# Optimization experiments

Measured on AMD Instinct MI355X. Metric: run time of the kernel, lower is better.

## Reference

```python
import jax, jax.numpy as jnp
import numpy as np

N_NODES = 20000
N_EDGES = 320000
C = 64  # classes
NEG_SLOPE = 0.2  # DGL GATConv default


def setup_inputs() -> dict:
    key = jax.random.key(0)
    ks = jax.random.split(key, 32)
    dims = [C, 2 * C, 4 * C, 8 * C, 16 * C]
    inp = {}
    inp["feat"] = jax.random.normal(ks[0], (N_NODES, C), jnp.float32)
    k = 1
    for i in range(4):
        din, dout = dims[i], dims[i + 1]
        scale = 1.0 / np.sqrt(din)
        inp[f"W{i+1}"] = jax.random.normal(ks[k], (din, dout), jnp.float32) * scale; k += 1
        inp[f"al{i+1}"] = jax.random.normal(ks[k], (dout,), jnp.float32) * 0.1; k += 1
        inp[f"ar{i+1}"] = jax.random.normal(ks[k], (dout,), jnp.float32) * 0.1; k += 1
        inp[f"b{i+1}"] = jnp.zeros((dout,), jnp.float32)
    inp["relW"] = jax.random.normal(ks[k], (16 * C, C), jnp.float32) * (1.0 / np.sqrt(16 * C)); k += 1
    inp["relB"] = jnp.zeros((C,), jnp.float32)
    inp["src"] = jax.random.randint(ks[k], (N_EDGES,), 0, N_NODES, jnp.int32); k += 1
    inp["dst"] = jax.random.randint(ks[k], (N_EDGES,), 0, N_NODES, jnp.int32); k += 1
    inp["rel"] = jnp.ones((C,), jnp.int32)
    inp["order"] = 1023
    return inp


def _gat_layer(x, W, al, ar, b, src, dst, n_nodes):
    """DGL GATConv (num_heads=1, allow_zero_in_degree=True, activation=tanh)."""
    h = x @ W                                   # [N, D] projected features
    el = h @ al                                 # [N] attn_l score per node
    er = h @ ar                                 # [N] attn_r score per node
    e = jax.nn.leaky_relu(el[src] + er[dst], NEG_SLOPE)          # [E]
    # segment (edge) softmax over incoming edges of each dst node
    m = jax.ops.segment_max(e, dst, num_segments=n_nodes)        # [N]
    ex = jnp.exp(e - m[dst])                                      # [E]
    s = jax.ops.segment_sum(ex, dst, num_segments=n_nodes)       # [N]
    alpha = ex / s[dst]                                           # [E]
    # gather neighbor messages, weight by attention, scatter-add to dst
    out = jax.ops.segment_sum(h[src] * alpha[:, None], dst, num_segments=n_nodes)  # [N, D]
    return jnp.tanh(out + b)


def reference(feat, W1, al1, ar1, b1, W2, al2, ar2, b2, W3, al3, ar3, b3,
              W4, al4, ar4, b4, relW, relB, src, dst, rel, order):
    n = feat.shape[0]
    h = _gat_layer(feat, W1, al1, ar1, b1, src, dst, n)
    h = _gat_layer(h, W2, al2, ar2, b2, src, dst, n)
    h = _gat_layer(h, W3, al3, ar3, b3, src, dst, n)
    h = _gat_layer(h, W4, al4, ar4, b4, src, dst, n)
    embeddings = h[: order + 1]                  # first order+1 node embeddings
    pooling = jnp.mean(embeddings, axis=0)       # [16C]
    logits = pooling @ relW + relB               # [C]
    nz = jnp.nonzero(rel, size=rel.shape[0])[0]  # static-size nonzero (rel is all-ones)
    return logits[nz]
```

## Files before the change

### kernel.cpp

```cpp
#include <hip/hip_runtime.h>
#include <hip/hip_bf16.h>

#define NN 20000
#define NE 320000
#define MPAD 20096
#define ORD 1024
#define NB 79

typedef __hip_bfloat16 bf16;
typedef __attribute__((ext_vector_type(8))) short bf16x8;
typedef __attribute__((ext_vector_type(4))) float f32x4;

#define SCOPE_AGENT __HIP_MEMORY_SCOPE_AGENT

static __device__ __forceinline__ float b2f(bf16 x) { return __bfloat162float(x); }
static __device__ __forceinline__ float bfbits2f(short s) {
    unsigned int u = ((unsigned int)(unsigned short)s) << 16;
    float f; __builtin_memcpy(&f, &u, 4); return f;
}
static __device__ __forceinline__ short f2bfbits(float v) {
    bf16 h = __float2bfloat16(v);
    short s; __builtin_memcpy(&s, &h, 2); return s;
}
static __device__ __forceinline__ unsigned short f2bfu(float v) {
    bf16 h = __float2bfloat16(v);
    unsigned short s; __builtin_memcpy(&s, &h, 2); return s;
}
static __device__ __forceinline__ float aloadf(const float* p) {
    return __hip_atomic_load(p, __ATOMIC_RELAXED, SCOPE_AGENT);
}

__global__ void setup_all(const float* __restrict__ feat,
                          const float* __restrict__ W1, const float* __restrict__ al1, const float* __restrict__ ar1,
                          const float* __restrict__ W2, const float* __restrict__ al2, const float* __restrict__ ar2,
                          const float* __restrict__ W3, const float* __restrict__ al3, const float* __restrict__ ar3,
                          const float* __restrict__ W4, const float* __restrict__ al4, const float* __restrict__ ar4,
                          bf16* __restrict__ featb, bf16* __restrict__ wt1,
                          bf16* __restrict__ wt2, bf16* __restrict__ wt3,
                          bf16* __restrict__ wt4, int* __restrict__ counts,
                          int* __restrict__ hglob,
                          float* __restrict__ walbuf, float* __restrict__ warbuf) {
    int b = blockIdx.x;
    if (b < 960) {
        const float *W, *al, *ar; int dout, k; float *wal, *war;
        if (b < 64)       { W = W1; al = al1; ar = ar1; dout = 128;  k = b;       wal = walbuf;        war = warbuf; }
        else if (b < 192) { W = W2; al = al2; ar = ar2; dout = 256;  k = b - 64;  wal = walbuf + 512;  war = warbuf + 512; }
        else if (b < 448) { W = W3; al = al3; ar = ar3; dout = 512;  k = b - 192; wal = walbuf + 1024; war = warbuf + 1024; }
        else              { W = W4; al = al4; ar = ar4; dout = 1024; k = b - 448; wal = walbuf + 1536; war = warbuf + 1536; }
        const float* row = W + (long)k * dout;
        float sl = 0.f, sr = 0.f;
        for (int j = threadIdx.x; j < dout; j += 256) {
            float w = row[j];
            sl += w * al[j];
            sr += w * ar[j];
        }
        __shared__ float sbl[256], sbr[256];
        sbl[threadIdx.x] = sl; sbr[threadIdx.x] = sr;
        __syncthreads();
        for (int st = 128; st > 0; st >>= 1) {
            if (threadIdx.x < st) {
                sbl[threadIdx.x] += sbl[threadIdx.x + st];
                sbr[threadIdx.x] += sbr[threadIdx.x + st];
            }
            __syncthreads();
        }
        if (threadIdx.x == 0) { wal[k] = sbl[0]; war[k] = sbr[0]; }
        return;
    }
    int i = (b - 960) * 256 + threadIdx.x;
    if (i < NN) counts[i] = 0;
    if (i < 256) hglob[i] = 0;
    if (i < 320000) {
        float4 f = *(const float4*)(feat + 4 * (long)i);
        ushort4 h;
        h.x = f2bfu(f.x); h.y = f2bfu(f.y); h.z = f2bfu(f.z); h.w = f2bfu(f.w);
        *(ushort4*)((unsigned short*)featb + 4 * (long)i) = h;
        return;
    }
    i -= 320000;
    if (i < 8192)  { int r = i >> 7,  c = i & 127;  wt1[c * 64 + r]  = __float2bfloat16(W1[i]); return; }
    i -= 8192;
    if (i < 32768) { int r = i >> 8,  c = i & 255;  wt2[c * 128 + r] = __float2bfloat16(W2[i]); return; }
    i -= 32768;
    if (i < 131072){ int r = i >> 9,  c = i & 511;  wt3[c * 256 + r] = __float2bfloat16(W3[i]); return; }
    i -= 131072;
    if (i < 524288){ int r = i >> 10, c = i & 1023; wt4[c * 512 + r] = __float2bfloat16(W4[i]); return; }
}

__global__ void hist_kernel(const int* __restrict__ dst, int* __restrict__ counts, int n) {
    int i = blockIdx.x * blockDim.x + threadIdx.x;
    if (i < n) atomicAdd(&counts[dst[i]], 1);
}

__global__ void csr_phase1(const int* __restrict__ counts, int* __restrict__ blocksums,
                           int* __restrict__ hglob) {
    __shared__ int sb[256];
    __shared__ int hh[256];
    int tid = threadIdx.x;
    hh[tid] = 0;
    int i = blockIdx.x * 256 + tid;
    int c = (i < NN) ? counts[i] : 0;
    sb[tid] = c;
    __syncthreads();
    for (int st = 128; st > 0; st >>= 1) {
        if (tid < st) sb[tid] += sb[tid + st];
        __syncthreads();
    }
    if (tid == 0) blocksums[blockIdx.x] = sb[0];
    if (i < NN) {
        int d = c > 255 ? 255 : c;
        atomicAdd(&hh[d], 1);
    }
    __syncthreads();
    if (hh[tid] > 0) atomicAdd(&hglob[tid], hh[tid]);
}

__global__ void csr_phase2(const int* __restrict__ counts, const int* __restrict__ blocksums,
                           int* __restrict__ offsets, int* __restrict__ cursor,
                           const int* __restrict__ hglob, int* __restrict__ curg) {
    int tid = threadIdx.x;
    if (blockIdx.x == NB) {
        __shared__ int hs[256];
        int orig = hglob[tid];
        hs[tid] = orig;
        __syncthreads();
        for (int st = 1; st < 256; st <<= 1) {
            int u = (tid >= st) ? hs[tid - st] : 0;
            __syncthreads();
            hs[tid] += u;
            __syncthreads();
        }
        curg[tid] = hs[tid] - orig;
        return;
    }
    __shared__ int bs[256];
    bs[tid] = (tid < NB) ? blocksums[tid] : 0;
    __syncthreads();
    for (int st = 1; st < 256; st <<= 1) {
        int u = (tid >= st) ? bs[tid - st] : 0;
        __syncthreads();
        bs[tid] += u;
        __syncthreads();
    }
    int base = (blockIdx.x == 0) ? 0 : bs[blockIdx.x - 1];
    __shared__ int sc[256];
    int i = blockIdx.x * 256 + tid;
    int c = (i < NN) ? counts[i] : 0;
    sc[tid] = c;
    __syncthreads();
    for (int st = 1; st < 256; st <<= 1) {
        int u = (tid >= st) ? sc[tid - st] : 0;
        __syncthreads();
        sc[tid] += u;
        __syncthreads();
    }
    int excl = base + sc[tid] - c;
    if (i < NN) { offsets[i] = excl; cursor[i] = excl; }
    if (i == NN - 1) offsets[NN] = excl + c;
}

__global__ void scatter_elr(const int* __restrict__ src, const int* __restrict__ dst,
                            int* __restrict__ cursor, int* __restrict__ esrc,
                            const int* __restrict__ counts, int* __restrict__ curg,
                            int* __restrict__ nodeperm,
                            const bf16* __restrict__ X, const float* __restrict__ wal,
                            const float* __restrict__ war, float* __restrict__ el,
                            float* __restrict__ er) {
    int b = blockIdx.x;
    if (b < 1250) {
        int i = b * 256 + threadIdx.x;
        int p = atomicAdd(&cursor[dst[i]], 1);
        esrc[p] = src[i];
        return;
    }
    if (b < 1250 + NB) {
        __shared__ int hh[256];
        __shared__ int basep[256];
        int tid = threadIdx.x;
        hh[tid] = 0;
        __syncthreads();
        int i = (b - 1250) * 256 + tid;
        int d = 0, rank = 0;
        bool valid = (i < NN);
        if (valid) {
            d = counts[i]; if (d > 255) d = 255;
            rank = atomicAdd(&hh[d], 1);
        }
        __syncthreads();
        if (hh[tid] > 0) basep[tid] = atomicAdd(&curg[tid], hh[tid]);
        __syncthreads();
        if (valid) nodeperm[basep[d] + rank] = i;
        return;
    }
    int idx = (b - 1250 - NB) * 256 + threadIdx.x;
    int node = idx >> 6;
    int lane = threadIdx.x & 63;
    if (node >= NN) return;
    float x = bfbits2f(*((const short*)X + (long)node * 64 + lane));
    float sl = x * wal[lane];
    float sr = x * war[lane];
    #pragma unroll
    for (int o = 32; o > 0; o >>= 1) {
        sl += __shfl_down(sl, o);
        sr += __shfl_down(sr, o);
    }
    if (lane == 0) { el[node] = sl; er[node] = sr; }
}

__global__ void aggregate_sm(const bf16* __restrict__ X,
                             const float* __restrict__ el, const float* __restrict__ er,
                             const int* __restrict__ esrc, const int* __restrict__ off,
                             const int* __restrict__ perm, float* __restrict__ zbuf, int zn,
                             bf16* __restrict__ Y, int din, int log2chunks, int nmax) {
    __shared__ __attribute__((aligned(16))) float alds[32][68];
    {
        int z = blockIdx.x * 256 + threadIdx.x;
        if (z < zn) zbuf[z] = 0.f;
    }
    int chunk = blockIdx.x & ((1 << log2chunks) - 1);
    int nb = blockIdx.x >> log2chunks;
    int sub = threadIdx.x >> 3, sl = threadIdx.x & 7;
    int slot = nb * 32 + sub;
    if (slot >= nmax) return;
    int node = perm ? perm[slot] : slot;
    int s = off[node], e = off[node + 1];
    int deg = e - s;
    bool fast = (deg <= 64);

    float erd = (deg > 0) ? er[node] : 0.f;
    float vmax = -1e30f, inv = 0.f;
    if (fast) {
        float v[8];
        #pragma unroll
        for (int t = 0; t < 8; t++) {
            v[t] = -1e30f;
            int idx = sl + 8 * t;
            if (idx < deg) {
                float x = el[esrc[s + idx]] + erd;
                v[t] = x >= 0.f ? x : 0.2f * x;
            }
            vmax = fmaxf(vmax, v[t]);
        }
        #pragma unroll
        for (int o = 1; o < 8; o <<= 1) vmax = fmaxf(vmax, __shfl_xor(vmax, o));
        float ssum = 0.f;
        #pragma unroll
        for (int t = 0; t < 8; t++) {
            int idx = sl + 8 * t;
            if (idx < deg) { v[t] = __expf(v[t] - vmax); ssum += v[t]; }
        }
        #pragma unroll
        for (int o = 1; o < 8; o <<= 1) ssum += __shfl_xor(ssum, o);
        inv = 1.f / ssum;
        #pragma unroll
        for (int t = 0; t < 8; t++) {
            int idx = sl + 8 * t;
            if (idx < deg) alds[sub][idx] = v[t] * inv;
        }
    } else {
        for (int j = s + sl; j < e; j += 8) {
            float x = el[esrc[j]] + erd;
            x = x >= 0.f ? x : 0.2f * x;
            vmax = fmaxf(vmax, x);
        }
        #pragma unroll
        for (int o = 1; o < 8; o <<= 1) vmax = fmaxf(vmax, __shfl_xor(vmax, o));
        float ssum = 0.f;
        for (int j = s + sl; j < e; j += 8) {
            float x = el[esrc[j]] + erd;
            x = x >= 0.f ? x : 0.2f * x;
            ssum += __expf(x - vmax);
        }
        #pragma unroll
        for (int o = 1; o < 8; o <<= 1) ssum += __shfl_xor(ssum, o);
        inv = 1.f / ssum;
    }

    const short* xb = (const short*)X + chunk * 64 + sl * 8;
    float acc[8] = {0.f,0.f,0.f,0.f,0.f,0.f,0.f,0.f};
    int j = s;
    if (fast) {
        for (; j + 8 <= e; j += 8) {
            int ofs = j - s;
            f32x4 a0 = *(const f32x4*)&alds[sub][ofs];
            f32x4 a1 = *(const f32x4*)&alds[sub][ofs + 4];
            int r[8]; bf16x8 w[8];
            #pragma unroll
            for (int q = 0; q < 8; q++) r[q] = esrc[j + q];
            #pragma unroll
            for (int q = 0; q < 8; q++) w[q] = *(const bf16x8*)(xb + (long)r[q] * din);
            #pragma unroll
            for (int q = 0; q < 4; q++)
                #pragma unroll
                for (int v = 0; v < 8; v++) acc[v] += a0[q] * bfbits2f(w[q][v]);
            #pragma unroll
            for (int q = 0; q < 4; q++)
                #pragma unroll
                for (int v = 0; v < 8; v++) acc[v] += a1[q] * bfbits2f(w[4 + q][v]);
        }
        for (; j + 4 <= e; j += 4) {
            int ofs = j - s;
            f32x4 a0 = *(const f32x4*)&alds[sub][ofs];
            int r[4]; bf16x8 w[4];
            #pragma unroll
            for (int q = 0; q < 4; q++) r[q] = esrc[j + q];
            #pragma unroll
            for (int q = 0; q < 4; q++) w[q] = *(const bf16x8*)(xb + (long)r[q] * din);
            #pragma unroll
            for (int q = 0; q < 4; q++)
                #pragma unroll
                for (int v = 0; v < 8; v++) acc[v] += a0[q] * bfbits2f(w[q][v]);
        }
        for (; j < e; j++) {
            float a = alds[sub][j - s];
            bf16x8 w = *(const bf16x8*)(xb + (long)esrc[j] * din);
            #pragma unroll
            for (int v = 0; v < 8; v++) acc[v] += a * bfbits2f(w[v]);
        }
    } else {
        for (; j + 8 <= e; j += 8) {
            int r[8]; float a[8]; bf16x8 w[8];
            #pragma unroll
            for (int q = 0; q < 8; q++) r[q] = esrc[j + q];
            #pragma unroll
            for (int q = 0; q < 8; q++) {
                float x = el[r[q]] + erd;
                x = x >= 0.f ? x : 0.2f * x;
                a[q] = __expf(x - vmax) * inv;
            }
            #pragma unroll
            for (int q = 0; q < 8; q++) w[q] = *(const bf16x8*)(xb + (long)r[q] * din);
            #pragma unroll
            for (int q = 0; q < 8; q++)
                #pragma unroll
                for (int v = 0; v < 8; v++) acc[v] += a[q] * bfbits2f(w[q][v]);
        }
        for (; j < e; j++) {
            int r = esrc[j];
            float x = el[r] + erd;
            x = x >= 0.f ? x : 0.2f * x;
            float a = __expf(x - vmax) * inv;
            bf16x8 w = *(const bf16x8*)(xb + (long)r * din);
            #pragma unroll
            for (int v = 0; v < 8; v++) acc[v] += a * bfbits2f(w[v]);
        }
    }
    short outv[8];
    #pragma unroll
    for (int v = 0; v < 8; v++) outv[v] = f2bfbits(acc[v]);
    bf16x8 store;
    __builtin_memcpy(&store, outv, sizeof(store));
    *(bf16x8*)((short*)Y + (long)node * din + chunk * 64 + sl * 8) = store;
}

__global__ __launch_bounds__(256, 4)
void gemm_k64(const bf16* __restrict__ A, const bf16* __restrict__ WT,
              const float* __restrict__ bias, bf16* __restrict__ C,
              const float* __restrict__ wal, const float* __restrict__ war,
              float* __restrict__ elp, float* __restrict__ erp) {
    int gw = blockIdx.x * 4 + (threadIdx.x >> 6);
    if (gw >= 2500) return;
    int r0 = (gw >> 1) << 4;
    int col0 = (gw & 1) << 6;
    int lane = threadIdx.x & 63;
    int m = lane & 15, quad = lane >> 4;

    const short* Ab = (const short*)A + (long)(r0 + m) * 64 + quad * 8;
    bf16x8 a0 = *(const bf16x8*)(Ab);
    bf16x8 a1 = *(const bf16x8*)(Ab + 32);

    f32x4 acc[4];
    bf16x8 b0[4], b1[4];
    #pragma unroll
    for (int t = 0; t < 4; t++) {
        acc[t] = (f32x4){0.f, 0.f, 0.f, 0.f};
        const short* Bb = (const short*)WT + (long)(col0 + t * 16 + m) * 64 + quad * 8;
        b0[t] = *(const bf16x8*)(Bb);
        b1[t] = *(const bf16x8*)(Bb + 32);
    }
    #pragma unroll
    for (int t = 0; t < 4; t++) {
        acc[t] = __builtin_amdgcn_mfma_f32_16x16x32_bf16(a0, b0[t], acc[t], 0, 0, 0);
        acc[t] = __builtin_amdgcn_mfma_f32_16x16x32_bf16(a1, b1[t], acc[t], 0, 0, 0);
    }

    float sl4[4] = {0.f, 0.f, 0.f, 0.f};
    float sr4[4] = {0.f, 0.f, 0.f, 0.f};
    #pragma unroll
    for (int t = 0; t < 4; t++) {
        int col = col0 + t * 16 + m;
        float bb = bias[col];
        float wl = wal[col], wrr = war[col];
        #pragma unroll
        for (int r = 0; r < 4; r++) {
            float v = tanhf(acc[t][r] + bb);
            sl4[r] += v * wl;
            sr4[r] += v * wrr;
            float vn = __shfl_xor(v, 1);
            if ((m & 1) == 0) {
                unsigned int pk = (unsigned int)f2bfu(v) | ((unsigned int)f2bfu(vn) << 16);
                int row = r0 + quad * 4 + r;
                *(unsigned int*)((short*)C + (long)row * 128 + col) = pk;
            }
        }
    }
    #pragma unroll
    for (int r = 0; r < 4; r++) {
        float s1 = sl4[r], s2 = sr4[r];
        #pragma unroll
        for (int o = 1; o < 16; o <<= 1) {
            s1 += __shfl_xor(s1, o);
            s2 += __shfl_xor(s2, o);
        }
        if (m == 0) {
            int row = r0 + quad * 4 + r;
            atomicAdd(&elp[row], s1);
            atomicAdd(&erp[row], s2);
        }
    }
}

__global__ __launch_bounds__(256, 4)
void gemm_tiled(const bf16* __restrict__ A, const bf16* __restrict__ WT,
                const float* __restrict__ bias, bf16* __restrict__ C,
                const float* __restrict__ wal, const float* __restrict__ war,
                float* __restrict__ elp, float* __restrict__ erp,
                float* __restrict__ poolacc,
                const float* __restrict__ relW, const float* __restrict__ relB,
                const int* __restrict__ order, const int* __restrict__ rel,
                float* __restrict__ headout,
                int M, int K, int N, int ncols, int nrows) {
    __shared__ short smem[16384];
    short* As = smem;
    short* Bs = smem + 8192;
    int g = blockIdx.x;
    int rowTile = ((g >> 3) / ncols) * 8 + (g & 7);
    int colTile = (g >> 3) % ncols;
    if (rowTile >= nrows) return;
    int row0 = rowTile << 7, col0 = colTile << 7;
    int tid = threadIdx.x;
    int lane = tid & 63, wave = tid >> 6;
    int wr = (wave >> 1) << 6;
    int wc = (wave & 1) << 6;
    int m = lane & 15, quad = lane >> 4;

    f32x4 acc[4][4];
    #pragma unroll
    for (int i = 0; i < 4; i++)
        #pragma unroll
        for (int j = 0; j < 4; j++) acc[i][j] = (f32x4){0.f, 0.f, 0.f, 0.f};

    const short* Ab = (const short*)A;
    const short* Bb = (const short*)WT;
    long ga[4], gb[4];
    #pragma unroll
    for (int n = 0; n < 4; n++) {
        int chunk = n * 256 + tid;
        int row = chunk >> 3;
        int qg = (chunk & 7) ^ (row & 7);
        ga[n] = (long)(row0 + row) * K + qg * 8;
        gb[n] = (long)(col0 + row) * K + qg * 8;
    }

    typedef const __attribute__((address_space(1))) void cgvoid;
    typedef __attribute__((address_space(3))) void lvoid;

    for (int k0 = 0; k0 < K; k0 += 64) {
        __syncthreads();
        #pragma unroll
        for (int n = 0; n < 4; n++)
            __builtin_amdgcn_global_load_lds((cgvoid*)(Ab + ga[n] + k0),
                                             (lvoid*)(As + (n * 256 + tid) * 8), 16, 0, 0);
        #pragma unroll
        for (int n = 0; n < 4; n++)
            __builtin_amdgcn_global_load_lds((cgvoid*)(Bb + gb[n] + k0),
                                             (lvoid*)(Bs + (n * 256 + tid) * 8), 16, 0, 0);
        __syncthreads();
        #pragma unroll
        for (int h = 0; h < 2; h++) {
            bf16x8 af[4], bfr[4];
            #pragma unroll
            for (int s = 0; s < 4; s++) {
                int ra = wr + s * 16 + m;
                int sa = (h * 4 + quad) ^ (ra & 7);
                af[s] = *(const bf16x8*)(As + ra * 64 + sa * 8);
                int rb = wc + s * 16 + m;
                int sb = (h * 4 + quad) ^ (rb & 7);
                bfr[s] = *(const bf16x8*)(Bs + rb * 64 + sb * 8);
            }
            #pragma unroll
            for (int i = 0; i < 4; i++)
                #pragma unroll
                for (int j = 0; j < 4; j++)
                    acc[i][j] = __builtin_amdgcn_mfma_f32_16x16x32_bf16(af[i], bfr[j], acc[i][j], 0, 0, 0);
        }
    }

    float bb[4], walr[4], warr[4];
    #pragma unroll
    for (int j = 0; j < 4; j++) {
        int col = col0 + wc + j * 16 + m;
        bb[j] = bias[col];
        if (elp) { walr[j] = wal[col]; warr[j] = war[col]; }
    }
    float colsum[4] = {0.f, 0.f, 0.f, 0.f};
    __syncthreads();
    short* myep = smem + wave * 1152;
    #pragma unroll
    for (int i = 0; i < 4; i++) {
        float sl4[4] = {0.f, 0.f, 0.f, 0.f};
        float sr4[4] = {0.f, 0.f, 0.f, 0.f};
        #pragma unroll
        for (int j = 0; j < 4; j++) {
            #pragma unroll
            for (int r = 0; r < 4; r++) {
                float v = tanhf(acc[i][j][r] + bb[j]);
                if (elp) { sl4[r] += v * walr[j]; sr4[r] += v * warr[j]; }
                if (poolacc) colsum[j] += v;
                float vn = __shfl_xor(v, 1);
                if ((m & 1) == 0) {
                    unsigned int pk = (unsigned int)f2bfu(v) | ((unsigned int)f2bfu(vn) << 16);
                    *(unsigned int*)(myep + (quad * 4 + r) * 72 + j * 16 + m) = pk;
                }
            }
        }
        #pragma unroll
        for (int pass = 0; pass < 2; pass++) {
            int lr = pass * 8 + (lane >> 3);
            int lc = (lane & 7) * 8;
            bf16x8 v = *(const bf16x8*)(myep + lr * 72 + lc);
            int row = row0 + wr + i * 16 + lr;
            if (row < M)
                *(bf16x8*)((short*)C + (long)row * N + col0 + wc + lc) = v;
        }
        if (elp) {
            #pragma unroll
            for (int r = 0; r < 4; r++) {
                float s1 = sl4[r], s2 = sr4[r];
                #pragma unroll
                for (int o = 1; o < 16; o <<= 1) {
                    s1 += __shfl_xor(s1, o);
                    s2 += __shfl_xor(s2, o);
                }
                if (m == 0) {
                    int row = row0 + wr + i * 16 + quad * 4 + r;
                    if (row < M) {
                        atomicAdd(&elp[row], s1);
                        atomicAdd(&erp[row], s2);
                    }
                }
            }
        }
    }
    if (poolacc) {
        #pragma unroll
        for (int j = 0; j < 4; j++) {
            float cs = colsum[j];
            cs += __shfl_xor(cs, 16);
            cs += __shfl_xor(cs, 32);
            if (quad == 0)
                atomicAdd(&poolacc[col0 + wc + j * 16 + m], cs);
        }
    }
    if (headout) {
        __syncthreads();
        __shared__ int lastf;
        if (tid == 0) {
            unsigned int old = __hip_atomic_fetch_add((unsigned int*)&poolacc[1024], 1u,
                                                      __ATOMIC_ACQ_REL, SCOPE_AGENT);
            lastf = (old == 63u) ? 1 : 0;
        }
        __syncthreads();
        if (!lastf) return;
        float* ps = (float*)smem;
        float (*part)[64] = (float(*)[64])(smem + 2048);
        for (int i = tid; i < 1024; i += 256) ps[i] = aloadf(&poolacc[i]);
        __syncthreads();
        int t = tid & 63, p = tid >> 6;
        const float* wp = relW + (long)p * 256 * 64 + t;
        float s = 0.f;
        #pragma unroll 8
        for (int c = 0; c < 256; c++) s += ps[p * 256 + c] * wp[(long)c * 64];
        part[p][t] = s;
        __syncthreads();
        if (tid < 64) {
            float rows = (float)(order[0] + 1);
            float lv = (part[0][tid] + part[1][tid] + part[2][tid] + part[3][tid]) / rows + relB[tid];
            int rv = rel[tid];
            unsigned long long mask = __ballot(rv != 0);
            int pos = __popcll(mask & ((1ULL << tid) - 1));
            int count = __popcll(mask);
            float l0 = __shfl(lv, 0);
            if (rv) headout[pos] = lv;
            if (tid >= count) headout[tid] = l0;
        }
    }
}

extern "C" void kernel_launch(void* const* d_in, const int* in_sizes, int n_in,
                              void* d_out, int out_size, void* d_ws, size_t ws_size,
                              hipStream_t stream) {
    const float* feat = (const float*)d_in[0];
    const float* W[4]  = {(const float*)d_in[1], (const float*)d_in[5], (const float*)d_in[9],  (const float*)d_in[13]};
    const float* al[4] = {(const float*)d_in[2], (const float*)d_in[6], (const float*)d_in[10], (const float*)d_in[14]};
    const float* ar[4] = {(const float*)d_in[3], (const float*)d_in[7], (const float*)d_in[11], (const float*)d_in[15]};
    const float* bias[4] = {(const float*)d_in[4], (const float*)d_in[8], (const float*)d_in[12], (const float*)d_in[16]};
    const float* relW = (const float*)d_in[17];
    const float* relB = (const float*)d_in[18];
    const int* src = (const int*)d_in[19];
    const int* dst = (const int*)d_in[20];
    const int* rel = (const int*)d_in[21];
    const int* order = (const int*)d_in[22];

    const int dims[5] = {64, 128, 256, 512, 1024};

    char* p = (char*)d_ws;
    auto carve = [&](size_t bytes) {
        void* r = (void*)p;
        p += (bytes + 255) & ~(size_t)255;
        return r;
    };
    bf16* xbuf = (bf16*)carve((size_t)MPAD * 1024 * sizeof(bf16));
    bf16* ybuf = (bf16*)carve((size_t)MPAD * 512 * sizeof(bf16));
    bf16* featb = (bf16*)carve((size_t)MPAD * 64 * sizeof(bf16));
    bf16* wt[4];
    for (int l = 0; l < 4; l++)
        wt[l] = (bf16*)carve((size_t)dims[l] * dims[l + 1] * sizeof(bf16));
    float* walbuf = (float*)carve(4 * 512 * sizeof(float));
    float* warbuf = (float*)carve(4 * 512 * sizeof(float));
    float* elbuf[2];
    elbuf[0] = (float*)carve((size_t)2 * NN * sizeof(float));
    elbuf[1] = (float*)carve((size_t)2 * NN * sizeof(float));
    int* counts  = (int*)carve((size_t)NN * sizeof(int));
    int* offsets = (int*)carve((size_t)(NN + 1) * sizeof(int));
    int* cursor  = (int*)carve((size_t)NN * sizeof(int));
    int* esrc    = (int*)carve((size_t)NE * sizeof(int));
    int* nodeperm = (int*)carve((size_t)NN * sizeof(int));
    int* blocksums = (int*)carve((size_t)NB * sizeof(int));
    int* hglob   = (int*)carve(256 * sizeof(int));
    int* curg    = (int*)carve(256 * sizeof(int));
    float* poolsum = (float*)carve(1056 * sizeof(float));

    setup_all<<<960 + 3970, 256, 0, stream>>>(
        feat, W[0], al[0], ar[0], W[1], al[1], ar[1],
        W[2], al[2], ar[2], W[3], al[3], ar[3],
        featb, wt[0], wt[1], wt[2], wt[3], counts, hglob, walbuf, warbuf);

    hist_kernel<<<(NE + 255) / 256, 256, 0, stream>>>(dst, counts, NE);
    csr_phase1<<<NB, 256, 0, stream>>>(counts, blocksums, hglob);
    csr_phase2<<<NB + 1, 256, 0, stream>>>(counts, blocksums, offsets, cursor, hglob, curg);
    scatter_elr<<<1250 + NB + 5000, 256, 0, stream>>>(src, dst, cursor, esrc,
                                                      counts, curg, nodeperm,
                                                      featb, walbuf, warbuf,
                                                      elbuf[0], elbuf[0] + NN);

    const bf16* x = featb;
    const int nrows = MPAD / 128;
    const int nrowsPad = 160;
    const int log2c[4] = {0, 1, 2, 3};
    for (int l = 0; l < 4; l++) {
        int K = dims[l], N = dims[l + 1];
        float* elr_rd = elbuf[l & 1];
        float* elr_wr = elbuf[(l + 1) & 1];
        int nmax  = (l < 3) ? NN : ORD;
        int nodeBlocks = (nmax + 31) / 32;
        const int* aggPerm = (l < 3) ? nodeperm : nullptr;
        float* zbuf = (l < 3) ? elr_wr : poolsum;
        int zn = (l < 3) ? 2 * NN : 1025;
        aggregate_sm<<<nodeBlocks << log2c[l], 256, 0, stream>>>(
            x, elr_rd, elr_rd + NN, esrc, offsets, aggPerm, zbuf, zn, ybuf, K, log2c[l], nmax);
        int ncols = N >> 7;
        if (l == 0) {
            gemm_k64<<<625, 256, 0, stream>>>(ybuf, wt[0], bias[0], xbuf,
                                              walbuf + 512, warbuf + 512,
                                              elr_wr, elr_wr + NN);
        } else if (l < 3) {
            gemm_tiled<<<nrowsPad * ncols, 256, 0, stream>>>(
                ybuf, wt[l], bias[l], xbuf,
                walbuf + (l + 1) * 512, warbuf + (l + 1) * 512,
                elr_wr, elr_wr + NN, nullptr,
                nullptr, nullptr, nullptr, nullptr, nullptr,
                NN, K, N, ncols, nrows);
        } else {
            gemm_tiled<<<8 * ncols, 256, 0, stream>>>(
                ybuf, wt[l], bias[l], xbuf,
                nullptr, nullptr, nullptr, nullptr, poolsum,
                relW, relB, order, rel, (float*)d_out,
                ORD, K, N, ncols, 8);
        }
        x = xbuf;
    }
}
```

Measured before the change: 286.9 us.

## Fuse layer-1 attention aggregation with K=64 GEMM into one kernel

Layer 1's edge-softmax aggregation and its 64x128 projection GEMM now run in a single kernel. The aggregated rows stay in swizzled shared memory and feed MFMA directly, and el/er are reduced in LDS instead of through global atomics. This removes one launch, the ybuf round trip to global memory, and the zeroing of the el/er buffers. In exchange the fused kernel drops the degree-sorted node permutation, so load balance depends on node order. It also assumes NN is a multiple of 32, and the host loop is unrolled into explicit launches.

```diff
diff --git a/kernel.cpp b/kernel.cpp
--- a/kernel.cpp
+++ b/kernel.cpp
@@ -207,6 +207,200 @@
     if (lane == 0) { el[node] = sl; er[node] = sr; }
 }
 
+__global__ __launch_bounds__(256, 4)
+void agg_gemm_l1(const bf16* __restrict__ X,
+                 const float* __restrict__ el, const float* __restrict__ er,
+                 const int* __restrict__ esrc, const int* __restrict__ off,
+                 const bf16* __restrict__ WT, const float* __restrict__ bias,
+                 bf16* __restrict__ C,
+                 const float* __restrict__ wal, const float* __restrict__ war,
+                 float* __restrict__ elo, float* __restrict__ ero) {
+    __shared__ __attribute__((aligned(16))) float alds[32][68];
+    __shared__ __attribute__((aligned(16))) short arow[32 * 64];
+    __shared__ float elds[2][32], erds[2][32];
+    int tid = threadIdx.x;
+    int sub = tid >> 3, sl = tid & 7;
+    int node0 = blockIdx.x << 5;
+    int node = node0 + sub;
+
+    int s = off[node], e = off[node + 1];
+    int deg = e - s;
+    bool fast = (deg <= 64);
+    float erd = (deg > 0) ? er[node] : 0.f;
+    float vmax = -1e30f, inv = 0.f;
+    if (fast) {
+        float v[8];
+        #pragma unroll
+        for (int t = 0; t < 8; t++) {
+            v[t] = -1e30f;
+            int idx = sl + 8 * t;
+            if (idx < deg) {
+                float x = el[esrc[s + idx]] + erd;
+                v[t] = x >= 0.f ? x : 0.2f * x;
+            }
+            vmax = fmaxf(vmax, v[t]);
+        }
+        #pragma unroll
+        for (int o = 1; o < 8; o <<= 1) vmax = fmaxf(vmax, __shfl_xor(vmax, o));
+        float ssum = 0.f;
+        #pragma unroll
+        for (int t = 0; t < 8; t++) {
+            int idx = sl + 8 * t;
+            if (idx < deg) { v[t] = __expf(v[t] - vmax); ssum += v[t]; }
+        }
+        #pragma unroll
+        for (int o = 1; o < 8; o <<= 1) ssum += __shfl_xor(ssum, o);
+        inv = 1.f / ssum;
+        #pragma unroll
+        for (int t = 0; t < 8; t++) {
+            int idx = sl + 8 * t;
+            if (idx < deg) alds[sub][idx] = v[t] * inv;
+        }
+    } else {
+        for (int j = s + sl; j < e; j += 8) {
+            float x = el[esrc[j]] + erd;
+            x = x >= 0.f ? x : 0.2f * x;
+            vmax = fmaxf(vmax, x);
+        }
+        #pragma unroll
+        for (int o = 1; o < 8; o <<= 1) vmax = fmaxf(vmax, __shfl_xor(vmax, o));
+        float ssum = 0.f;
+        for (int j = s + sl; j < e; j += 8) {
+            float x = el[esrc[j]] + erd;
+            x = x >= 0.f ? x : 0.2f * x;
+            ssum += __expf(x - vmax);
+        }
+        #pragma unroll
+        for (int o = 1; o < 8; o <<= 1) ssum += __shfl_xor(ssum, o);
+        inv = 1.f / ssum;
+    }
+    const short* xb = (const short*)X + sl * 8;
+    float acc[8] = {0.f,0.f,0.f,0.f,0.f,0.f,0.f,0.f};
+    int j = s;
+    if (fast) {
+        for (; j + 8 <= e; j += 8) {
+            int ofs = j - s;
+            f32x4 a0 = *(const f32x4*)&alds[sub][ofs];
+            f32x4 a1 = *(const f32x4*)&alds[sub][ofs + 4];
+            int r[8]; bf16x8 w[8];
+            #pragma unroll
+            for (int q = 0; q < 8; q++) r[q] = esrc[j + q];
+            #pragma unroll
+            for (int q = 0; q < 8; q++) w[q] = *(const bf16x8*)(xb + (long)r[q] * 64);
+            #pragma unroll
+            for (int q = 0; q < 4; q++)
+                #pragma unroll
+                for (int v = 0; v < 8; v++) acc[v] += a0[q] * bfbits2f(w[q][v]);
+            #pragma unroll
+            for (int q = 0; q < 4; q++)
+                #pragma unroll
+                for (int v = 0; v < 8; v++) acc[v] += a1[q] * bfbits2f(w[4 + q][v]);
+        }
+        for (; j + 4 <= e; j += 4) {
+            int ofs = j - s;
+            f32x4 a0 = *(const f32x4*)&alds[sub][ofs];
+            int r[4]; bf16x8 w[4];
+            #pragma unroll
+            for (int q = 0; q < 4; q++) r[q] = esrc[j + q];
+            #pragma unroll
+            for (int q = 0; q < 4; q++) w[q] = *(const bf16x8*)(xb + (long)r[q] * 64);
+            #pragma unroll
+            for (int q = 0; q < 4; q++)
+                #pragma unroll
+                for (int v = 0; v < 8; v++) acc[v] += a0[q] * bfbits2f(w[q][v]);
+        }
+        for (; j < e; j++) {
+            float a = alds[sub][j - s];
+            bf16x8 w = *(const bf16x8*)(xb + (long)esrc[j] * 64);
+            #pragma unroll
+            for (int v = 0; v < 8; v++) acc[v] += a * bfbits2f(w[v]);
+        }
+    } else {
+        for (; j < e; j++) {
+            int r = esrc[j];
+            float x = el[r] + erd;
+            x = x >= 0.f ? x : 0.2f * x;
+            float a = __expf(x - vmax) * inv;
+            bf16x8 w = *(const bf16x8*)(xb + (long)r * 64);
+            #pragma unroll
+            for (int v = 0; v < 8; v++) acc[v] += a * bfbits2f(w[v]);
+        }
+    }
+    {
+        short outv[8];
+        #pragma unroll
+        for (int v = 0; v < 8; v++) outv[v] = f2bfbits(acc[v]);
+        bf16x8 st;
+        __builtin_memcpy(&st, outv, sizeof(st));
+        int qs = sl ^ (sub & 7);
+        *(bf16x8*)(arow + sub * 64 + qs * 8) = st;
+    }
+    __syncthreads();
+
+    int lane = tid & 63, wave = tid >> 6;
+    int r0 = (wave >> 1) << 4;
+    int col0 = (wave & 1) << 6;
+    int m = lane & 15, quad = lane >> 4;
+    int rr = r0 + m;
+    bf16x8 a0 = *(const bf16x8*)(arow + rr * 64 + ((quad ^ (rr & 7)) * 8));
+    bf16x8 a1 = *(const bf16x8*)(arow + rr * 64 + (((quad + 4) ^ (rr & 7)) * 8));
+
+    f32x4 gacc[4];
+    bf16x8 b0[4], b1[4];
+    #pragma unroll
+    for (int t = 0; t < 4; t++) {
+        gacc[t] = (f32x4){0.f, 0.f, 0.f, 0.f};
+        const short* Bb = (const short*)WT + (long)(col0 + t * 16 + m) * 64 + quad * 8;
+        b0[t] = *(const bf16x8*)(Bb);
+        b1[t] = *(const bf16x8*)(Bb + 32);
+    }
+    #pragma unroll
+    for (int t = 0; t < 4; t++) {
+        gacc[t] = __builtin_amdgcn_mfma_f32_16x16x32_bf16(a0, b0[t], gacc[t], 0, 0, 0);
+        gacc[t] = __builtin_amdgcn_mfma_f32_16x16x32_bf16(a1, b1[t], gacc[t], 0, 0, 0);
+    }
+
+    float sl4[4] = {0.f, 0.f, 0.f, 0.f};
+    float sr4[4] = {0.f, 0.f, 0.f, 0.f};
+    #pragma unroll
+    for (int t = 0; t < 4; t++) {
+        int col = col0 + t * 16 + m;
+        float bb = bias[col];
+        float wl = wal[col], wrr = war[col];
+        #pragma unroll
+        for (int r = 0; r < 4; r++) {
+            float v = tanhf(gacc[t][r] + bb);
+            sl4[r] += v * wl;
+            sr4[r] += v * wrr;
+            float vn = __shfl_xor(v, 1);
+            if ((m & 1) == 0) {
+                unsigned int pk = (unsigned int)f2bfu(v) | ((unsigned int)f2bfu(vn) << 16);
+                int row = node0 + r0 + quad * 4 + r;
+                *(unsigned int*)((short*)C + (long)row * 128 + col) = pk;
+            }
+        }
+    }
+    #pragma unroll
+    for (int r = 0; r < 4; r++) {
+        float s1 = sl4[r], s2 = sr4[r];
+        #pragma unroll
+        for (int o = 1; o < 16; o <<= 1) {
+            s1 += __shfl_xor(s1, o);
+            s2 += __shfl_xor(s2, o);
+        }
+        if (m == 0) {
+            int lr = r0 + quad * 4 + r;
+            elds[wave & 1][lr] = s1;
+            erds[wave & 1][lr] = s2;
+        }
+    }
+    __syncthreads();
+    if (tid < 32) {
+        elo[node0 + tid] = elds[0][tid] + elds[1][tid];
+        ero[node0 + tid] = erds[0][tid] + erds[1][tid];
+    }
+}
+
 __global__ void aggregate_sm(const bf16* __restrict__ X,
                              const float* __restrict__ el, const float* __restrict__ er,
                              const int* __restrict__ esrc, const int* __restrict__ off,
@@ -351,73 +545,6 @@
     bf16x8 store;
     __builtin_memcpy(&store, outv, sizeof(store));
     *(bf16x8*)((short*)Y + (long)node * din + chunk * 64 + sl * 8) = store;
-}
-
-__global__ __launch_bounds__(256, 4)
-void gemm_k64(const bf16* __restrict__ A, const bf16* __restrict__ WT,
-              const float* __restrict__ bias, bf16* __restrict__ C,
-              const float* __restrict__ wal, const float* __restrict__ war,
-              float* __restrict__ elp, float* __restrict__ erp) {
-    int gw = blockIdx.x * 4 + (threadIdx.x >> 6);
-    if (gw >= 2500) return;
-    int r0 = (gw >> 1) << 4;
-    int col0 = (gw & 1) << 6;
-    int lane = threadIdx.x & 63;
-    int m = lane & 15, quad = lane >> 4;
-
-    const short* Ab = (const short*)A + (long)(r0 + m) * 64 + quad * 8;
-    bf16x8 a0 = *(const bf16x8*)(Ab);
-    bf16x8 a1 = *(const bf16x8*)(Ab + 32);
-
-    f32x4 acc[4];
-    bf16x8 b0[4], b1[4];
-    #pragma unroll
-    for (int t = 0; t < 4; t++) {
-        acc[t] = (f32x4){0.f, 0.f, 0.f, 0.f};
-        const short* Bb = (const short*)WT + (long)(col0 + t * 16 + m) * 64 + quad * 8;
-        b0[t] = *(const bf16x8*)(Bb);
-        b1[t] = *(const bf16x8*)(Bb + 32);
-    }
-    #pragma unroll
-    for (int t = 0; t < 4; t++) {
-        acc[t] = __builtin_amdgcn_mfma_f32_16x16x32_bf16(a0, b0[t], acc[t], 0, 0, 0);
-        acc[t] = __builtin_amdgcn_mfma_f32_16x16x32_bf16(a1, b1[t], acc[t], 0, 0, 0);
-    }
-
-    float sl4[4] = {0.f, 0.f, 0.f, 0.f};
-    float sr4[4] = {0.f, 0.f, 0.f, 0.f};
-    #pragma unroll
-    for (int t = 0; t < 4; t++) {
-        int col = col0 + t * 16 + m;
-        float bb = bias[col];
-        float wl = wal[col], wrr = war[col];
-        #pragma unroll
-        for (int r = 0; r < 4; r++) {
-            float v = tanhf(acc[t][r] + bb);
-            sl4[r] += v * wl;
-            sr4[r] += v * wrr;
-            float vn = __shfl_xor(v, 1);
-            if ((m & 1) == 0) {
-                unsigned int pk = (unsigned int)f2bfu(v) | ((unsigned int)f2bfu(vn) << 16);
-                int row = r0 + quad * 4 + r;
-                *(unsigned int*)((short*)C + (long)row * 128 + col) = pk;
-            }
-        }
-    }
-    #pragma unroll
-    for (int r = 0; r < 4; r++) {
-        float s1 = sl4[r], s2 = sr4[r];
-        #pragma unroll
-        for (int o = 1; o < 16; o <<= 1) {
-            s1 += __shfl_xor(s1, o);
-            s2 += __shfl_xor(s2, o);
-        }
-        if (m == 0) {
-            int row = r0 + quad * 4 + r;
-            atomicAdd(&elp[row], s1);
-            atomicAdd(&erp[row], s2);
-        }
-    }
 }
 
 __global__ __launch_bounds__(256, 4)
@@ -654,40 +781,31 @@
                                                       featb, walbuf, warbuf,
                                                       elbuf[0], elbuf[0] + NN);
 
-    const bf16* x = featb;
-    const int nrows = MPAD / 128;
-    const int nrowsPad = 160;
-    const int log2c[4] = {0, 1, 2, 3};
-    for (int l = 0; l < 4; l++) {
-        int K = dims[l], N = dims[l + 1];
-        float* elr_rd = elbuf[l & 1];
-        float* elr_wr = elbuf[(l + 1) & 1];
-        int nmax  = (l < 3) ? NN : ORD;
-        int nodeBlocks = (nmax + 31) / 32;
-        const int* aggPerm = (l < 3) ? nodeperm : nullptr;
-        float* zbuf = (l < 3) ? elr_wr : poolsum;
-        int zn = (l < 3) ? 2 * NN : 1025;
-        aggregate_sm<<<nodeBlocks << log2c[l], 256, 0, stream>>>(
-            x, elr_rd, elr_rd + NN, esrc, offsets, aggPerm, zbuf, zn, ybuf, K, log2c[l], nmax);
-        int ncols = N >> 7;
-        if (l == 0) {
-            gemm_k64<<<625, 256, 0, stream>>>(ybuf, wt[0], bias[0], xbuf,
-                                              walbuf + 512, warbuf + 512,
-                                              elr_wr, elr_wr + NN);
-        } else if (l < 3) {
-            gemm_tiled<<<nrowsPad * ncols, 256, 0, stream>>>(
-                ybuf, wt[l], bias[l], xbuf,
-                walbuf + (l + 1) * 512, warbuf + (l + 1) * 512,
-                elr_wr, elr_wr + NN, nullptr,
-                nullptr, nullptr, nullptr, nullptr, nullptr,
-                NN, K, N, ncols, nrows);
-        } else {
-            gemm_tiled<<<8 * ncols, 256, 0, stream>>>(
-                ybuf, wt[l], bias[l], xbuf,
-                nullptr, nullptr, nullptr, nullptr, poolsum,
-                relW, relB, order, rel, (float*)d_out,
-                ORD, K, N, ncols, 8);
-        }
-        x = xbuf;
-    }
-}
+    agg_gemm_l1<<<625, 256, 0, stream>>>(featb, elbuf[0], elbuf[0] + NN, esrc, offsets,
+                                         wt[0], bias[0], xbuf,
+                                         walbuf + 512, warbuf + 512,
+                                         elbuf[1], elbuf[1] + NN);
+
+    aggregate_sm<<<1250, 256, 0, stream>>>(xbuf, elbuf[1], elbuf[1] + NN, esrc, offsets,
+                                           nodeperm, elbuf[0], 2 * NN, ybuf, 128, 1, NN);
+    gemm_tiled<<<160 * 2, 256, 0, stream>>>(ybuf, wt[1], bias[1], xbuf,
+                                            walbuf + 1024, warbuf + 1024,
+                                            elbuf[0], elbuf[0] + NN, nullptr,
+                                            nullptr, nullptr, nullptr, nullptr, nullptr,
+                                            NN, 128, 256, 2, 157);
+
+    aggregate_sm<<<2500, 256, 0, stream>>>(xbuf, elbuf[0], elbuf[0] + NN, esrc, offsets,
+                                           nodeperm, elbuf[1], 2 * NN, ybuf, 256, 2, NN);
+    gemm_tiled<<<160 * 4, 256, 0, stream>>>(ybuf, wt[2], bias[2], xbuf,
+                                            walbuf + 1536, warbuf + 1536,
+                                            elbuf[1], elbuf[1] + NN, nullptr,
+                                            nullptr, nullptr, nullptr, nullptr, nullptr,
+                                            NN, 256, 512, 4, 157);
+
+    aggregate_sm<<<32 << 3, 256, 0, stream>>>(xbuf, elbuf[1], elbuf[1] + NN, esrc, offsets,
+                                              nullptr, poolsum, 1025, ybuf, 512, 3, ORD);
+    gemm_tiled<<<8 * 8, 256, 0, stream>>>(ybuf, wt[3], bias[3], xbuf,
+                                          nullptr, nullptr, nullptr, nullptr, poolsum,
+                                          relW, relB, order, rel, (float*)d_out,
+                                          ORD, 512, 1024, 8, 8);
+}
```

New measurement: 283.3 us. About the same (-1.2%).
